# Optimization experiments

Measured on AMD Instinct MI355X. Metric: run time of the kernel, lower is better.

Reference implementation:

```python
import jax, jax.numpy as jnp
import numpy as np

B, E, L, D = 64, 32, 512, 768
C1 = 1024
C2 = 1024
H = 8
EG = 32768
SPAN_H = 512
NLAB = 4


def setup_inputs() -> dict:
    key = jax.random.key(0)
    ks = jax.random.split(key, 48)
    def w(i, shape, s=0.02):
        return s * jax.random.normal(ks[i], shape, jnp.float32)
    N = B * E
    inp = {}
    inp['last_hidden'] = jax.random.normal(ks[0], (B, L, D), jnp.float32)
    mask = (jax.random.uniform(ks[1], (B, E, L)) < 0.25).astype(jnp.float32)
    inp['batch_edu_mask'] = mask.at[:, :, 0].set(1.0)  # every EDU has >=1 token
    inp['edu_lengths'] = jax.random.randint(ks[2], (B,), 1, E + 1)
    inp['batch_edge'] = jax.random.randint(ks[3], (2, EG), 0, N)
    inp['batch_edge_type'] = jax.random.randint(ks[4], (EG, 1), 0, 5).astype(jnp.float32)
    inp['batch_is_main'] = jax.random.randint(ks[5], (EG, 1), 0, 2).astype(jnp.float32)
    # span attention MLP
    inp['W1'] = w(6, (D, SPAN_H)); inp['b1'] = jnp.zeros((SPAN_H,), jnp.float32)
    inp['W2'] = w(7, (SPAN_H, 1)); inp['b2'] = jnp.zeros((1,), jnp.float32)
    # edge-attr embeddings (Linear(1, C))
    inp['Wr1'] = w(8, (1, C1)); inp['br1'] = jnp.zeros((C1,), jnp.float32)
    inp['Wm1'] = w(9, (1, C1)); inp['bm1'] = jnp.zeros((C1,), jnp.float32)
    inp['Wr2'] = w(10, (1, C2)); inp['br2'] = jnp.zeros((C2,), jnp.float32)
    inp['Wm2'] = w(11, (1, C2)); inp['bm2'] = jnp.zeros((C2,), jnp.float32)
    # TransformerConv 1: in=D, heads*out=C1, edge_dim=C1
    inp['q1W'] = w(12, (D, C1)); inp['q1b'] = jnp.zeros((C1,), jnp.float32)
    inp['k1W'] = w(13, (D, C1)); inp['k1b'] = jnp.zeros((C1,), jnp.float32)
    inp['v1W'] = w(14, (D, C1)); inp['v1b'] = jnp.zeros((C1,), jnp.float32)
    inp['e1W'] = w(15, (C1, C1))
    inp['s1W'] = w(16, (D, C1)); inp['s1b'] = jnp.zeros((C1,), jnp.float32)
    # TransformerConv 2: in=C1, heads*out=C2, edge_dim=C2
    inp['q2W'] = w(17, (C1, C2)); inp['q2b'] = jnp.zeros((C2,), jnp.float32)
    inp['k2W'] = w(18, (C1, C2)); inp['k2b'] = jnp.zeros((C2,), jnp.float32)
    inp['v2W'] = w(19, (C1, C2)); inp['v2b'] = jnp.zeros((C2,), jnp.float32)
    inp['e2W'] = w(20, (C2, C2))
    inp['s2W'] = w(21, (C1, C2)); inp['s2b'] = jnp.zeros((C2,), jnp.float32)
    inp['fcW'] = w(22, (C2, NLAB)); inp['fcb'] = jnp.zeros((NLAB,), jnp.float32)
    return inp


def _tconv(x, src, dst, edge_attr, Wq, bq, Wk, bk, Wv, bv, We, Ws, bs):
    # PyG TransformerConv (concat=True, beta=False, root_weight=True)
    N = x.shape[0]
    C = Wq.shape[1]
    d = C // H
    q = (x @ Wq + bq).reshape(N, H, d)              # [N,H,d]
    e = (edge_attr @ We).reshape(-1, H, d)          # [Eg,H,d] (lin_edge has no bias)
    k = (x @ Wk + bk)[src].reshape(-1, H, d) + e    # [Eg,H,d]
    v = (x @ Wv + bv)[src].reshape(-1, H, d) + e    # [Eg,H,d]
    logits = (q[dst] * k).sum(-1) / jnp.sqrt(jnp.float32(d))  # [Eg,H]
    m = jax.ops.segment_max(logits, dst, num_segments=N)
    ex = jnp.exp(logits - m[dst])
    den = jax.ops.segment_sum(ex, dst, num_segments=N)
    alpha = ex / den[dst]                            # scatter-softmax over dst
    agg = jax.ops.segment_sum(v * alpha[:, :, None], dst, num_segments=N).reshape(N, C)
    return agg + x @ Ws + bs                         # skip connection


def reference(last_hidden, batch_edu_mask, edu_lengths, batch_edge, batch_edge_type, batch_is_main,
              W1, b1, W2, b2,
              Wr1, br1, Wm1, bm1, Wr2, br2, Wm2, bm2,
              q1W, q1b, k1W, k1b, v1W, v1b, e1W, s1W, s1b,
              q2W, q2b, k2W, k2b, v2W, v2b, e2W, s2W, s2b,
              fcW, fcb):
    b = last_hidden.shape[0]
    # span extractor: masked softmax attention pooling per EDU
    att = jnp.maximum(last_hidden @ W1 + b1, 0.0) @ W2 + b2      # [B,L,1]
    logits = jnp.swapaxes(att, 1, 2) - 1e5 * (1.0 - batch_edu_mask)  # [B,E,L]
    probs = jax.nn.softmax(logits, axis=-1)
    edu = probs @ last_hidden                                     # [B,E,D]
    node = edu.reshape(-1, edu.shape[-1])                         # [B*E,D]
    src, dst = batch_edge[0], batch_edge[1]
    ea1 = batch_edge_type @ Wr1 + br1 + batch_is_main @ Wm1 + bm1
    node = _tconv(node, src, dst, ea1, q1W, q1b, k1W, k1b, v1W, v1b, e1W, s1W, s1b)
    ea2 = batch_edge_type @ Wr2 + br2 + batch_is_main @ Wm2 + bm2
    node = _tconv(node, src, dst, ea2, q2W, q2b, k2W, k2b, v2W, v2b, e2W, s2W, s2b)
    node = node.reshape(b, -1, node.shape[-1])                    # [B,E,C2]
    last_du = node[jnp.arange(b), edu_lengths - 1]                # [B,C2]
    return last_du @ fcW + fcb                                    # [B,NLAB]
```

## Files before the change

### kernel.cpp

```cpp
#include <hip/hip_runtime.h>
#include <math.h>
#include <stdint.h>

#define B_  64
#define E_  32
#define L_  512
#define D_  768
#define C_  1024
#define H_  8
#define EG_ 32768
#define SH_ 512
#define N_  2048
#define ND_ (N_ * D_)

typedef __bf16 bf16x8 __attribute__((ext_vector_type(8)));
typedef float f32x4 __attribute__((ext_vector_type(4)));
typedef unsigned short u16;
typedef u16 u16x4 __attribute__((ext_vector_type(4)));


__device__ __forceinline__ u16 bf16_rn(float x) {
  unsigned u = __builtin_bit_cast(unsigned, x);
  unsigned r = u + 0x7FFFu + ((u >> 16) & 1u);
  return (u16)(r >> 16);
}

__device__ __forceinline__ void gload16(const void* g, void* l) {
  __builtin_amdgcn_global_load_lds(
      (const __attribute__((address_space(1))) void*)(unsigned long long)(uintptr_t)g,
      (__attribute__((address_space(3))) void*)(unsigned int)(uintptr_t)l,
      16, 0, 0);
}

__global__ void k_wt9(const float* __restrict__ s0, const float* __restrict__ s1,
                      const float* __restrict__ s2, const float* __restrict__ s3,
                      const float* __restrict__ s4, const float* __restrict__ s5,
                      const float* __restrict__ s6, const float* __restrict__ s7,
                      const float* __restrict__ s8, u16* __restrict__ dstBase) {
  int x = blockIdx.x;
  const float* W; u16* TH; int K, Nc;
  if (x < 384) {
    W = s0; TH = dstBase; K = D_; Nc = SH_;
  } else if (x < 384 + 4 * 768) {
    int i = (x - 384) / 768; x = (x - 384) % 768;
    W = (i == 0) ? s1 : (i == 1) ? s2 : (i == 2) ? s3 : s4;
    TH = dstBase + SH_ * D_ + (size_t)i * C_ * D_; K = D_; Nc = C_;
  } else {
    int i = (x - 3456) / 1024; x = (x - 3456) % 1024;
    W = (i == 0) ? s5 : (i == 1) ? s6 : (i == 2) ? s7 : s8;
    TH = dstBase + SH_ * D_ + 4 * (size_t)C_ * D_ + (size_t)i * C_ * C_; K = C_; Nc = C_;
  }
  __shared__ float Ts[32][33];
  int nbk = K >> 5;
  int bk = x % nbk, bn = x / nbk;
  int tid = threadIdx.x;
  int tx = tid & 31, ty = tid >> 5;
  for (int r = ty; r < 32; r += 8)
    Ts[r][tx] = W[(size_t)(bk * 32 + r) * Nc + bn * 32 + tx];
  __syncthreads();
  for (int r = ty; r < 32; r += 8) {
    float v = Ts[tx][r];
    TH[(size_t)(bn * 32 + r) * K + bk * 32 + tx] = bf16_rn(v);
  }
}

__device__ __forceinline__ void gemm_core(
    const float* __restrict__ X, const u16* __restrict__ Bt,
    int K, int row0, int col0,
    u16* Ah, u16* Bh, f32x4 acc[4][4])
{
  int tid = threadIdx.x;
  int lane = tid & 63, w = tid >> 6;

  int aoff[4], boff[4];
#pragma unroll
  for (int i = 0; i < 4; i++) {
    int kc = lane >> 4;
    int rT = (w & 1) * 64 + i * 16 + (lane & 15);
    aoff[i] = rT * 128 + (((kc ^ (rT & 7)) & 7) << 4);
    int cT = (w >> 1) * 64 + i * 16 + (lane & 15);
    boff[i] = cT * 128 + (((kc ^ (cT & 7)) & 7) << 4);
  }

  int nkt = K >> 6;
  for (int kt = 0; kt < nkt; kt++) {
    int k0 = kt << 6;
    if (kt) __syncthreads();
#pragma unroll
    for (int p = 0; p < 8; p++) {
      int idx = tid + p * 256;
      int r = idx >> 4, c4 = idx & 15;
      float4 v = *(const float4*)&X[(size_t)(row0 + r) * K + k0 + c4 * 4];
      u16x4 hv = {bf16_rn(v.x), bf16_rn(v.y), bf16_rn(v.z), bf16_rn(v.w)};
      int off = r * 128 + ((((c4 >> 1) ^ (r & 7)) & 7) << 4) + (c4 & 1) * 8;
      *(u16x4*)((char*)Ah + off) = hv;
    }
#pragma unroll
    for (int q = 0; q < 4; q++) {
      int rT = w * 32 + q * 8 + (lane >> 3);
      int cs = (lane & 7) ^ (rT & 7);
      size_t gb = (size_t)(col0 + rT) * K + k0 + cs * 8;
      int lb = (w * 32 + q * 8) * 64;
      gload16(&Bt[gb], &Bh[lb]);
    }
    __syncthreads();
    bf16x8 ah0[4], ah1[4];
#pragma unroll
    for (int i = 0; i < 4; i++) {
      ah0[i] = *(const bf16x8*)((const char*)Ah + aoff[i]);
      ah1[i] = *(const bf16x8*)((const char*)Ah + (aoff[i] ^ 64));
    }
#pragma unroll
    for (int j = 0; j < 4; j++) {
      bf16x8 bh0 = *(const bf16x8*)((const char*)Bh + boff[j]);
#pragma unroll
      for (int i = 0; i < 4; i++)
        acc[i][j] = __builtin_amdgcn_mfma_f32_16x16x32_bf16(ah0[i], bh0, acc[i][j], 0, 0, 0);
      bf16x8 bh1 = *(const bf16x8*)((const char*)Bh + (boff[j] ^ 64));
#pragma unroll
      for (int i = 0; i < 4; i++)
        acc[i][j] = __builtin_amdgcn_mfma_f32_16x16x32_bf16(ah1[i], bh1, acc[i][j], 0, 0, 0);
    }
  }
}

__global__ __launch_bounds__(256) void k_span_m(
    const float* __restrict__ lh, const u16* __restrict__ W1t,
    const float* __restrict__ b1, const float* __restrict__ W2,
    float* __restrict__ att8) {
  __shared__ __align__(16) u16 Ah[128 * 64], Bh[128 * 64];
  int rb = blockIdx.x & 255, cb = blockIdx.x >> 8;
  int row0 = rb * 128, col0 = cb * 128;
  f32x4 acc[4][4];
#pragma unroll
  for (int i = 0; i < 4; i++)
#pragma unroll
    for (int j = 0; j < 4; j++) acc[i][j] = (f32x4){0.f, 0.f, 0.f, 0.f};
  gemm_core(lh, W1t, D_, row0, col0, Ah, Bh, acc);

  int lane = threadIdx.x & 63, w = threadIdx.x >> 6;
  int wrow = (w & 1) * 64, wcol = (w >> 1) * 64;
  float b1v[4], w2v[4];
#pragma unroll
  for (int j = 0; j < 4; j++) {
    int col = col0 + wcol + j * 16 + (lane & 15);
    b1v[j] = b1[col]; w2v[j] = W2[col];
  }
  float* dst = att8 + (size_t)(cb * 2 + (w >> 1)) * 32768;
#pragma unroll
  for (int i = 0; i < 4; i++) {
#pragma unroll
    for (int r = 0; r < 4; r++) {
      float s = 0.f;
#pragma unroll
      for (int j = 0; j < 4; j++) {
        float h = acc[i][j][r] + b1v[j];
        s += fmaxf(h, 0.f) * w2v[j];
      }
      s += __shfl_xor(s, 1); s += __shfl_xor(s, 2);
      s += __shfl_xor(s, 4); s += __shfl_xor(s, 8);
      if ((lane & 15) == 0)
        dst[row0 + wrow + i * 16 + (lane >> 4) * 4 + r] = s;
    }
  }
}

__global__ void k_probs(const float* __restrict__ att8, const float* __restrict__ b2,
                        const float* __restrict__ mask, float* __restrict__ pr) {
  int bi = blockIdx.x >> 2, eg = blockIdx.x & 3;
  int tid = threadIdx.x, lane = tid & 63, w = tid >> 6;
  __shared__ float att_s[512];
  float b2v = b2[0];
  int r0 = bi * 512 + tid;
  float s0 = b2v, s1 = b2v;
#pragma unroll
  for (int p = 0; p < 8; p++) {
    s0 += att8[(size_t)p * 32768 + r0];
    s1 += att8[(size_t)p * 32768 + r0 + 256];
  }
  att_s[tid] = s0;
  att_s[tid + 256] = s1;
  __syncthreads();
#pragma unroll
  for (int it = 0; it < 2; it++) {
    int e = eg * 8 + it * 4 + w;
    const float* mrow = &mask[(size_t)(bi * E_ + e) * L_];
    float4 m0 = *(const float4*)&mrow[lane * 8];
    float4 m1 = *(const float4*)&mrow[lane * 8 + 4];
    float4 a0 = *(const float4*)&att_s[lane * 8];
    float4 a1 = *(const float4*)&att_s[lane * 8 + 4];
    float v[8];
    v[0] = a0.x - 1e5f * (1.f - m0.x); v[1] = a0.y - 1e5f * (1.f - m0.y);
    v[2] = a0.z - 1e5f * (1.f - m0.z); v[3] = a0.w - 1e5f * (1.f - m0.w);
    v[4] = a1.x - 1e5f * (1.f - m1.x); v[5] = a1.y - 1e5f * (1.f - m1.y);
    v[6] = a1.z - 1e5f * (1.f - m1.z); v[7] = a1.w - 1e5f * (1.f - m1.w);
    float mx = v[0];
#pragma unroll
    for (int i = 1; i < 8; i++) mx = fmaxf(mx, v[i]);
#pragma unroll
    for (int o = 32; o; o >>= 1) mx = fmaxf(mx, __shfl_xor(mx, o));
    float s = 0.f;
#pragma unroll
    for (int i = 0; i < 8; i++) { v[i] = expf(v[i] - mx); s += v[i]; }
#pragma unroll
    for (int o = 32; o; o >>= 1) s += __shfl_xor(s, o);
    float inv = 1.f / s;
    float4 o0 = {v[0] * inv, v[1] * inv, v[2] * inv, v[3] * inv};
    float4 o1 = {v[4] * inv, v[5] * inv, v[6] * inv, v[7] * inv};
    float* prow = &pr[(size_t)(bi * E_ + e) * L_];
    *(float4*)&prow[lane * 8] = o0;
    *(float4*)&prow[lane * 8 + 4] = o1;
  }
}

__global__ __launch_bounds__(256) void k_pool_m(const float* __restrict__ lh,
    const float* __restrict__ pr, float* __restrict__ node0) {
  __shared__ __align__(16) u16 As[32 * 32];
  __shared__ __align__(16) u16 Bs[32 * 128];
  int bi = blockIdx.x / 6, dc = blockIdx.x % 6;
  int col0 = dc * 128;
  int tid = threadIdx.x, lane = tid & 63, w = tid >> 6;
  const float* lhb = lh + (size_t)bi * L_ * D_;
  const float* prb = pr + (size_t)bi * E_ * L_;

  f32x4 acc[2][2];
#pragma unroll
  for (int m = 0; m < 2; m++)
#pragma unroll
    for (int c = 0; c < 2; c++) acc[m][c] = (f32x4){0.f, 0.f, 0.f, 0.f};

  int aoff[2];
#pragma unroll
  for (int m = 0; m < 2; m++) {
    int kc = lane >> 4;
    int e = m * 16 + (lane & 15);
    aoff[m] = e * 64 + (((kc ^ ((e >> 1) & 3)) & 3) << 4);
  }
  int se = tid >> 3, sk4 = tid & 7;
  int saoff = se * 64 + ((((sk4 >> 1) ^ ((se >> 1) & 3)) & 3) << 4) + (sk4 & 1) * 8;

  for (int kt = 0; kt < 16; kt++) {
    int l0 = kt << 5;
    if (kt) __syncthreads();
    {
      float4 v = *(const float4*)&prb[(size_t)se * L_ + l0 + sk4 * 4];
      u16x4 hv = {bf16_rn(v.x), bf16_rn(v.y), bf16_rn(v.z), bf16_rn(v.w)};
      *(u16x4*)((char*)As + saoff) = hv;
    }
#pragma unroll
    for (int p = 0; p < 4; p++) {
      int idx = tid + p * 256;
      int k = idx >> 5, c4 = idx & 31;
      float4 v = *(const float4*)&lhb[(size_t)(l0 + k) * D_ + col0 + c4 * 4];
      u16x4 hv = {bf16_rn(v.x), bf16_rn(v.y), bf16_rn(v.z), bf16_rn(v.w)};
      *(u16x4*)&Bs[k * 128 + c4 * 4] = hv;
    }
    __syncthreads();
    bf16x8 af[2];
#pragma unroll
    for (int m = 0; m < 2; m++)
      af[m] = *(const bf16x8*)((const char*)As + aoff[m]);
#pragma unroll
    for (int c = 0; c < 2; c++) {
      int colT = w * 32 + c * 16 + (lane & 15);
      int kg = (lane >> 4) * 8;
      union { bf16x8 v; u16 u[8]; } bb;
#pragma unroll
      for (int j = 0; j < 8; j++) bb.u[j] = Bs[(kg + j) * 128 + colT];
#pragma unroll
      for (int m = 0; m < 2; m++)
        acc[m][c] = __builtin_amdgcn_mfma_f32_16x16x32_bf16(af[m], bb.v, acc[m][c], 0, 0, 0);
    }
  }
#pragma unroll
  for (int m = 0; m < 2; m++)
#pragma unroll
    for (int c = 0; c < 2; c++) {
      int col = col0 + w * 32 + c * 16 + (lane & 15);
#pragma unroll
      for (int r = 0; r < 4; r++) {
        int e = m * 16 + (lane >> 4) * 4 + r;
        node0[(size_t)(bi * E_ + e) * D_ + col] = acc[m][c][r];
      }
    }
}

__global__ __launch_bounds__(256) void k_gemm4_m(
    const float* __restrict__ X, int K,
    const u16* __restrict__ Wt,
    const float* __restrict__ bb0, const float* __restrict__ bb1,
    const float* __restrict__ bb2, const float* __restrict__ bb3,
    float* __restrict__ O0, float* __restrict__ O1,
    float* __restrict__ O2, float* __restrict__ O3) {
  __shared__ __align__(16) u16 Ah[128 * 64], Bh[128 * 64];
  int rb = blockIdx.x & 15, cbm = blockIdx.x >> 4;
  int mat = cbm >> 3;
  int col0 = (cbm & 7) * 128, row0 = rb * 128;
  const u16* Bt = Wt + (size_t)mat * C_ * K;
  const float* bias; float* O;
  if (mat == 0)      { bias = bb0; O = O0; }
  else if (mat == 1) { bias = bb1; O = O1; }
  else if (mat == 2) { bias = bb2; O = O2; }
  else               { bias = bb3; O = O3; }

  f32x4 acc[4][4];
#pragma unroll
  for (int i = 0; i < 4; i++)
#pragma unroll
    for (int j = 0; j < 4; j++) acc[i][j] = (f32x4){0.f, 0.f, 0.f, 0.f};
  gemm_core(X, Bt, K, row0, col0, Ah, Bh, acc);

  int lane = threadIdx.x & 63, w = threadIdx.x >> 6;
  int wrow = (w & 1) * 64, wcol = (w >> 1) * 64;
#pragma unroll
  for (int j = 0; j < 4; j++) {
    int col = col0 + wcol + j * 16 + (lane & 15);
    float bv = bias[col];
#pragma unroll
    for (int i = 0; i < 4; i++) {
      int rowb = row0 + wrow + i * 16 + (lane >> 4) * 4;
#pragma unroll
      for (int r = 0; r < 4; r++)
        O[(size_t)(rowb + r) * C_ + col] = acc[i][j][r] + bv;
    }
  }
}

__global__ void k_combo2(const float* __restrict__ Wr1, const float* __restrict__ br1,
                         const float* __restrict__ Wm1, const float* __restrict__ bm1,
                         const float* __restrict__ e1W,
                         const float* __restrict__ Wr2, const float* __restrict__ br2,
                         const float* __restrict__ Wm2, const float* __restrict__ bm2,
                         const float* __restrict__ e2W,
                         float* __restrict__ e1c, float* __restrict__ e2c) {
  int x = blockIdx.x;
  int conv = x >> 6;
  int jb = x & 3, kb = (x >> 2) & 15;
  const float *Wr, *br, *Wm, *bm, *eW; float* out;
  if (conv == 0) { Wr = Wr1; br = br1; Wm = Wm1; bm = bm1; eW = e1W; out = e1c; }
  else           { Wr = Wr2; br = br2; Wm = Wm2; bm = bm2; eW = e2W; out = e2c; }
  int tid = threadIdx.x;
  __shared__ float sw[3][64];
  int k0 = kb * 64;
  if (tid < 64) {
    sw[0][tid] = Wr[k0 + tid];
    sw[1][tid] = Wm[k0 + tid];
    sw[2][tid] = br[k0 + tid] + bm[k0 + tid];
  }
  __syncthreads();
  int j = jb * 256 + tid;
  float a0 = 0.f, a1 = 0.f, a2 = 0.f;
#pragma unroll 8
  for (int kk = 0; kk < 64; kk++) {
    float w = eW[(size_t)(k0 + kk) * C_ + j];
    a0 += sw[0][kk] * w; a1 += sw[1][kk] * w; a2 += sw[2][kk] * w;
  }
#pragma unroll
  for (int c = 0; c < 10; c++)
    atomicAdd(&out[c * C_ + j], (float)(c >> 1) * a0 + (float)(c & 1) * a1 + a2);
}

__global__ void k_count(const int* __restrict__ dst, int* __restrict__ cnt) {
  int eg = blockIdx.x * 256 + threadIdx.x;
  atomicAdd(&cnt[dst[eg]], 1);
}

__global__ void k_scan(const int* __restrict__ cnt, int* __restrict__ off) {
  __shared__ int part[256];
  int t = threadIdx.x;
  int local[8]; int s = 0;
#pragma unroll
  for (int i = 0; i < 8; i++) { local[i] = cnt[t * 8 + i]; s += local[i]; }
  part[t] = s;
  __syncthreads();
  if (t == 0) {
    int r = 0;
    for (int i = 0; i < 256; i++) { int v = part[i]; part[i] = r; r += v; }
    off[N_] = r;
  }
  __syncthreads();
  int r = part[t];
#pragma unroll
  for (int i = 0; i < 8; i++) { off[t * 8 + i] = r; r += local[i]; }
}

__global__ void k_scatter(const int* __restrict__ dst, int* __restrict__ wcnt,
                          const int* __restrict__ off, int* __restrict__ perm) {
  int eg = blockIdx.x * 256 + threadIdx.x;
  int d = dst[eg];
  int p = atomicAdd(&wcnt[d], 1);
  perm[off[d] + p] = eg;
}

__global__ void k_agg(const float* __restrict__ q, const float* __restrict__ k,
                      const float* __restrict__ v, const float* __restrict__ ec,
                      const int* __restrict__ srcA, const float* __restrict__ etype,
                      const float* __restrict__ emain, const int* __restrict__ off,
                      const int* __restrict__ perm, float* __restrict__ O) {
  int dst = blockIdx.x;
  int beg = off[dst];
  int cntE = off[dst + 1] - beg;
  if (cntE == 0) return;
  if (cntE > 128) cntE = 128;
  int tid = threadIdx.x;
  __shared__ float lg[128][8];
  __shared__ int srcs[128];
  __shared__ int cids[128];
  for (int e = tid; e < cntE; e += 256) {
    int eg = perm[beg + e];
    srcs[e] = srcA[eg];
    cids[e] = ((int)(etype[eg] + 0.5f)) * 2 + (int)(emain[eg] + 0.5f);
  }
  __syncthreads();
  int c = tid * 4;
  int h = tid >> 5;
  float4 qv = *(const float4*)&q[dst * C_ + c];
  const float scale = 0.08838834764831845f;
  for (int e = 0; e < cntE; e++) {
    int s = srcs[e], ci = cids[e];
    float4 kv = *(const float4*)&k[s * C_ + c];
    float4 ev = *(const float4*)&ec[ci * C_ + c];
    float p = qv.x * (kv.x + ev.x) + qv.y * (kv.y + ev.y) +
              qv.z * (kv.z + ev.z) + qv.w * (kv.w + ev.w);
#pragma unroll
    for (int o = 16; o; o >>= 1) p += __shfl_xor(p, o);
    if ((tid & 31) == 0) lg[e][h] = p * scale;
  }
  __syncthreads();
  if (tid < 8) {
    float m = -1e30f;
    for (int e = 0; e < cntE; e++) m = fmaxf(m, lg[e][tid]);
    float ssum = 0.f;
    for (int e = 0; e < cntE; e++) { float x = expf(lg[e][tid] - m); lg[e][tid] = x; ssum += x; }
    float inv = 1.f / ssum;
    for (int e = 0; e < cntE; e++) lg[e][tid] *= inv;
  }
  __syncthreads();
  float4 acc = {0.f, 0.f, 0.f, 0.f};
  for (int e = 0; e < cntE; e++) {
    float a = lg[e][h];
    int s = srcs[e], ci = cids[e];
    float4 vv = *(const float4*)&v[s * C_ + c];
    float4 ev = *(const float4*)&ec[ci * C_ + c];
    acc.x += a * (vv.x + ev.x); acc.y += a * (vv.y + ev.y);
    acc.z += a * (vv.z + ev.z); acc.w += a * (vv.w + ev.w);
  }
  float4 o = *(const float4*)&O[dst * C_ + c];
  o.x += acc.x; o.y += acc.y; o.z += acc.z; o.w += acc.w;
  *(float4*)&O[dst * C_ + c] = o;
}

__global__ void k_final(const float* __restrict__ nB, const int* __restrict__ lens,
                        const float* __restrict__ fcW, const float* __restrict__ fcb,
                        float* __restrict__ out) {
  int b = blockIdx.x;
  int idx = lens[b] - 1;
  const float* row = &nB[(b * E_ + idx) * C_];
  int tid = threadIdx.x;
  int c = tid * 4;
  float4 r = *(const float4*)&row[c];
  float4 w0 = *(const float4*)&fcW[(c + 0) * 4];
  float4 w1 = *(const float4*)&fcW[(c + 1) * 4];
  float4 w2 = *(const float4*)&fcW[(c + 2) * 4];
  float4 w3 = *(const float4*)&fcW[(c + 3) * 4];
  float p0 = r.x * w0.x + r.y * w1.x + r.z * w2.x + r.w * w3.x;
  float p1 = r.x * w0.y + r.y * w1.y + r.z * w2.y + r.w * w3.y;
  float p2 = r.x * w0.z + r.y * w1.z + r.z * w2.z + r.w * w3.z;
  float p3 = r.x * w0.w + r.y * w1.w + r.z * w2.w + r.w * w3.w;
#pragma unroll
  for (int o = 32; o; o >>= 1) {
    p0 += __shfl_xor(p0, o); p1 += __shfl_xor(p1, o);
    p2 += __shfl_xor(p2, o); p3 += __shfl_xor(p3, o);
  }
  __shared__ float red[4][4];
  if ((tid & 63) == 0) {
    int w = tid >> 6;
    red[w][0] = p0; red[w][1] = p1; red[w][2] = p2; red[w][3] = p3;
  }
  __syncthreads();
  if (tid == 0) {
#pragma unroll
    for (int j = 0; j < 4; j++)
      out[b * 4 + j] = red[0][j] + red[1][j] + red[2][j] + red[3][j] + fcb[j];
  }
}

extern "C" void kernel_launch(void* const* d_in, const int* in_sizes, int n_in,
                              void* d_out, int out_size, void* d_ws, size_t ws_size,
                              hipStream_t stream) {
  (void)in_sizes; (void)n_in; (void)out_size; (void)ws_size;
  const float* lh    = (const float*)d_in[0];
  const float* mask  = (const float*)d_in[1];
  const int*   lens  = (const int*)d_in[2];
  const int*   edge  = (const int*)d_in[3];
  const float* etype = (const float*)d_in[4];
  const float* emain = (const float*)d_in[5];
  const float* W1   = (const float*)d_in[6];
  const float* b1   = (const float*)d_in[7];
  const float* W2   = (const float*)d_in[8];
  const float* b2   = (const float*)d_in[9];
  const float* Wr1  = (const float*)d_in[10];
  const float* br1  = (const float*)d_in[11];
  const float* Wm1  = (const float*)d_in[12];
  const float* bm1  = (const float*)d_in[13];
  const float* Wr2  = (const float*)d_in[14];
  const float* br2  = (const float*)d_in[15];
  const float* Wm2  = (const float*)d_in[16];
  const float* bm2  = (const float*)d_in[17];
  const float* q1W  = (const float*)d_in[18];
  const float* q1b  = (const float*)d_in[19];
  const float* k1W  = (const float*)d_in[20];
  const float* k1b  = (const float*)d_in[21];
  const float* v1W  = (const float*)d_in[22];
  const float* v1b  = (const float*)d_in[23];
  const float* e1W  = (const float*)d_in[24];
  const float* s1W  = (const float*)d_in[25];
  const float* s1b  = (const float*)d_in[26];
  const float* q2W  = (const float*)d_in[27];
  const float* q2b  = (const float*)d_in[28];
  const float* k2W  = (const float*)d_in[29];
  const float* k2b  = (const float*)d_in[30];
  const float* v2W  = (const float*)d_in[31];
  const float* v2b  = (const float*)d_in[32];
  const float* e2W  = (const float*)d_in[33];
  const float* s2W  = (const float*)d_in[34];
  const float* s2b  = (const float*)d_in[35];
  const float* fcW  = (const float*)d_in[36];
  const float* fcb  = (const float*)d_in[37];

  float* ws    = (float*)d_ws;
  float* att   = ws;
  float* node0 = att + 32768;
  float* e1c   = node0 + ND_;
  float* e2c   = e1c + 10 * 1024;
  float* qb    = e2c + 10 * 1024;
  float* kb    = qb + N_ * C_;
  float* vb    = kb + N_ * C_;
  float* nA    = vb + N_ * C_;
  float* nBuf  = nA + N_ * C_;
  int* cnt  = (int*)(nBuf + N_ * C_);
  int* wcnt = cnt + N_;
  int* off  = wcnt + N_;
  int* perm = off + (N_ + 8);
  u16* wtb  = (u16*)(perm + EG_);
  u16* w1t  = wtb;
  u16* wt1  = w1t + SH_ * D_;
  u16* wt2  = wt1 + 4 * C_ * D_;

  float* pr   = qb;
  float* att8 = kb;

  const int* srcA = edge;
  const int* dstA = edge + EG_;

  (void)hipMemsetAsync(cnt, 0, 2 * N_ * sizeof(int), stream);
  k_count<<<EG_ / 256, 256, 0, stream>>>(dstA, cnt);
  k_scan<<<1, 256, 0, stream>>>(cnt, off);
  k_scatter<<<EG_ / 256, 256, 0, stream>>>(dstA, wcnt, off, perm);

  k_wt9<<<384 + 4 * 768 + 4 * 1024, 256, 0, stream>>>(
      W1, q1W, k1W, v1W, s1W, q2W, k2W, v2W, s2W, wtb);

  k_span_m<<<1024, 256, 0, stream>>>(lh, w1t, b1, W2, att8);

  (void)hipMemsetAsync(e1c, 0, 20 * C_ * sizeof(float), stream);
  k_combo2<<<128, 256, 0, stream>>>(Wr1, br1, Wm1, bm1, e1W,
                                    Wr2, br2, Wm2, bm2, e2W, e1c, e2c);

  k_probs<<<256, 256, 0, stream>>>(att8, b2, mask, pr);
  k_pool_m<<<384, 256, 0, stream>>>(lh, pr, node0);

  k_gemm4_m<<<512, 256, 0, stream>>>(node0, D_, wt1,
                                     q1b, k1b, v1b, s1b, qb, kb, vb, nA);
  k_agg<<<N_, 256, 0, stream>>>(qb, kb, vb, e1c, srcA, etype, emain, off, perm, nA);

  k_gemm4_m<<<512, 256, 0, stream>>>(nA, C_, wt2,
                                     q2b, k2b, v2b, s2b, qb, kb, vb, nBuf);
  k_agg<<<N_, 256, 0, stream>>>(qb, kb, vb, e2c, srcA, etype, emain, off, perm, nBuf);

  k_final<<<B_, 256, 0, stream>>>(nBuf, lens, fcW, fcb, (float*)d_out);
}
```

Baseline: 256.5 us.

## Compute full span-MLP hidden width per block and reduce partials in shared memory

The span attention GEMM now uses 512-thread blocks that each cover 128 rows and all 512 hidden columns. The fp32 activations are converted to bf16 once per row tile instead of being reloaded for each of the four column blocks. The per-wave ReLU·W2 partial sums are reduced in shared memory and written as a single att vector, so k_probs no longer sums 8 partial buffers. The cost is a larger per-block LDS footprint, twice the accumulator registers (4x8 tiles), and only 256 blocks, which lowers parallelism.

New measurement: 251.3 us. 2.0% less time.

```diff
diff --git a/kernel.cpp b/kernel.cpp
--- a/kernel.cpp
+++ b/kernel.cpp
@@ -124,62 +124,113 @@
   }
 }
 
-__global__ __launch_bounds__(256) void k_span_m(
+__global__ __launch_bounds__(512, 2) void k_span_m(
     const float* __restrict__ lh, const u16* __restrict__ W1t,
     const float* __restrict__ b1, const float* __restrict__ W2,
-    float* __restrict__ att8) {
-  __shared__ __align__(16) u16 Ah[128 * 64], Bh[128 * 64];
-  int rb = blockIdx.x & 255, cb = blockIdx.x >> 8;
-  int row0 = rb * 128, col0 = cb * 128;
-  f32x4 acc[4][4];
+    float* __restrict__ att) {
+  __shared__ __align__(16) u16 Ah[128 * 64];
+  __shared__ __align__(16) u16 Bh[512 * 64];
+  int row0 = blockIdx.x * 128;
+  int tid = threadIdx.x, lane = tid & 63, w = tid >> 6;
+  int rh = w & 1, cq = w >> 1;
+
+  f32x4 acc[4][8];
 #pragma unroll
   for (int i = 0; i < 4; i++)
 #pragma unroll
-    for (int j = 0; j < 4; j++) acc[i][j] = (f32x4){0.f, 0.f, 0.f, 0.f};
-  gemm_core(lh, W1t, D_, row0, col0, Ah, Bh, acc);
-
-  int lane = threadIdx.x & 63, w = threadIdx.x >> 6;
-  int wrow = (w & 1) * 64, wcol = (w >> 1) * 64;
-  float b1v[4], w2v[4];
-#pragma unroll
-  for (int j = 0; j < 4; j++) {
-    int col = col0 + wcol + j * 16 + (lane & 15);
+    for (int j = 0; j < 8; j++) acc[i][j] = (f32x4){0.f, 0.f, 0.f, 0.f};
+
+  int kc = lane >> 4;
+  int aoff[4], boff[8];
+#pragma unroll
+  for (int i = 0; i < 4; i++) {
+    int rT = rh * 64 + i * 16 + (lane & 15);
+    aoff[i] = rT * 128 + (((kc ^ (rT & 7)) & 7) << 4);
+  }
+#pragma unroll
+  for (int j = 0; j < 8; j++) {
+    int cT = cq * 128 + j * 16 + (lane & 15);
+    boff[j] = cT * 128 + (((kc ^ (cT & 7)) & 7) << 4);
+  }
+
+  for (int kt = 0; kt < 12; kt++) {
+    int k0 = kt << 6;
+    if (kt) __syncthreads();
+#pragma unroll
+    for (int p = 0; p < 4; p++) {
+      int idx = tid + p * 512;
+      int r = idx >> 4, c4 = idx & 15;
+      float4 v = *(const float4*)&lh[(size_t)(row0 + r) * D_ + k0 + c4 * 4];
+      u16x4 hv = {bf16_rn(v.x), bf16_rn(v.y), bf16_rn(v.z), bf16_rn(v.w)};
+      int off = r * 128 + ((((c4 >> 1) ^ (r & 7)) & 7) << 4) + (c4 & 1) * 8;
+      *(u16x4*)((char*)Ah + off) = hv;
+    }
+#pragma unroll
+    for (int q = 0; q < 8; q++) {
+      int rT = w * 64 + q * 8 + (lane >> 3);
+      int cs = (lane & 7) ^ (rT & 7);
+      size_t gb = (size_t)rT * D_ + k0 + cs * 8;
+      int lb = (w * 64 + q * 8) * 64;
+      gload16(&W1t[gb], &Bh[lb]);
+    }
+    __syncthreads();
+    bf16x8 ah0[4], ah1[4];
+#pragma unroll
+    for (int i = 0; i < 4; i++) {
+      ah0[i] = *(const bf16x8*)((const char*)Ah + aoff[i]);
+      ah1[i] = *(const bf16x8*)((const char*)Ah + (aoff[i] ^ 64));
+    }
+#pragma unroll
+    for (int j = 0; j < 8; j++) {
+      bf16x8 bh0 = *(const bf16x8*)((const char*)Bh + boff[j]);
+#pragma unroll
+      for (int i = 0; i < 4; i++)
+        acc[i][j] = __builtin_amdgcn_mfma_f32_16x16x32_bf16(ah0[i], bh0, acc[i][j], 0, 0, 0);
+      bf16x8 bh1 = *(const bf16x8*)((const char*)Bh + (boff[j] ^ 64));
+#pragma unroll
+      for (int i = 0; i < 4; i++)
+        acc[i][j] = __builtin_amdgcn_mfma_f32_16x16x32_bf16(ah1[i], bh1, acc[i][j], 0, 0, 0);
+    }
+  }
+
+  float b1v[8], w2v[8];
+#pragma unroll
+  for (int j = 0; j < 8; j++) {
+    int col = cq * 128 + j * 16 + (lane & 15);
     b1v[j] = b1[col]; w2v[j] = W2[col];
   }
-  float* dst = att8 + (size_t)(cb * 2 + (w >> 1)) * 32768;
+  __syncthreads();
+  float* sred = (float*)Ah;
 #pragma unroll
   for (int i = 0; i < 4; i++) {
 #pragma unroll
     for (int r = 0; r < 4; r++) {
       float s = 0.f;
 #pragma unroll
-      for (int j = 0; j < 4; j++) {
+      for (int j = 0; j < 8; j++) {
         float h = acc[i][j][r] + b1v[j];
         s += fmaxf(h, 0.f) * w2v[j];
       }
       s += __shfl_xor(s, 1); s += __shfl_xor(s, 2);
       s += __shfl_xor(s, 4); s += __shfl_xor(s, 8);
       if ((lane & 15) == 0)
-        dst[row0 + wrow + i * 16 + (lane >> 4) * 4 + r] = s;
-    }
-  }
-}
-
-__global__ void k_probs(const float* __restrict__ att8, const float* __restrict__ b2,
+        sred[cq * 128 + rh * 64 + i * 16 + (lane >> 4) * 4 + r] = s;
+    }
+  }
+  __syncthreads();
+  if (tid < 128)
+    att[row0 + tid] = sred[tid] + sred[128 + tid] + sred[256 + tid] + sred[384 + tid];
+}
+
+__global__ void k_probs(const float* __restrict__ att, const float* __restrict__ b2,
                         const float* __restrict__ mask, float* __restrict__ pr) {
   int bi = blockIdx.x >> 2, eg = blockIdx.x & 3;
   int tid = threadIdx.x, lane = tid & 63, w = tid >> 6;
   __shared__ float att_s[512];
   float b2v = b2[0];
   int r0 = bi * 512 + tid;
-  float s0 = b2v, s1 = b2v;
-#pragma unroll
-  for (int p = 0; p < 8; p++) {
-    s0 += att8[(size_t)p * 32768 + r0];
-    s1 += att8[(size_t)p * 32768 + r0 + 256];
-  }
-  att_s[tid] = s0;
-  att_s[tid + 256] = s1;
+  att_s[tid] = att[r0] + b2v;
+  att_s[tid + 256] = att[r0 + 256] + b2v;
   __syncthreads();
 #pragma unroll
   for (int it = 0; it < 2; it++) {
@@ -548,7 +599,6 @@
   u16* wt2  = wt1 + 4 * C_ * D_;
 
   float* pr   = qb;
-  float* att8 = kb;
 
   const int* srcA = edge;
   const int* dstA = edge + EG_;
@@ -561,13 +611,13 @@
   k_wt9<<<384 + 4 * 768 + 4 * 1024, 256, 0, stream>>>(
       W1, q1W, k1W, v1W, s1W, q2W, k2W, v2W, s2W, wtb);
 
-  k_span_m<<<1024, 256, 0, stream>>>(lh, w1t, b1, W2, att8);
+  k_span_m<<<256, 512, 0, stream>>>(lh, w1t, b1, W2, att);
 
   (void)hipMemsetAsync(e1c, 0, 20 * C_ * sizeof(float), stream);
   k_combo2<<<128, 256, 0, stream>>>(Wr1, br1, Wm1, bm1, e1W,
                                     Wr2, br2, Wm2, bm2, e2W, e1c, e2c);
 
-  k_probs<<<256, 256, 0, stream>>>(att8, b2, mask, pr);
+  k_probs<<<256, 256, 0, stream>>>(att, b2, mask, pr);
   k_pool_m<<<384, 256, 0, stream>>>(lh, pr, node0);
 
   k_gemm4_m<<<512, 256, 0, stream>>>(node0, D_, wt1,
```
